# Kernel optimization log

Measured on AMD Instinct MI355X. Metric: run time of the kernel, lower is better.

The kernel has to match this reference:

```python
import jax, jax.numpy as jnp
import numpy as np

L = 8      # subsequence_len
A = 4      # alphabet_size
D = 256    # sketch_dim
SEQ = 16384


def setup_inputs() -> dict:
    key = jax.random.key(0)
    k1, k2, k3 = jax.random.split(key, 3)
    sequence = jax.random.randint(k1, (SEQ,), 0, A)
    # stacked nn.Embedding weights: (L, A, D), init N(0, 0.5)
    hash_emb = 0.5 * jax.random.normal(k2, (L, A, D), dtype=jnp.float32)
    sign_logits = 0.5 * jax.random.normal(k3, (L, A), dtype=jnp.float32)
    return {"sequence": sequence, "hash_emb": hash_emb, "sign_logits": sign_logits}


def _forward(sequence, hash_emb, sign_logits):
    # roll_idx[j, s] = (j - s) % D  so that gather reproduces torch.roll(t, s)[j] = t[(j - s) % D]
    roll_idx = (jnp.arange(D)[:, None] - jnp.arange(D)[None, :]) % D
    p_arr = jnp.arange(1, L + 1, dtype=jnp.float32)           # p = 1..L
    Tp0 = jnp.zeros((L + 1, D), dtype=jnp.float32).at[0, 0].set(1.0)
    Tm0 = jnp.zeros((L + 1, D), dtype=jnp.float32)

    def step(carry, xs):
        Tp, Tm = carry                                         # (L+1, D) each
        c, i = xs
        valid = (c >= 0) & (c < A)
        c_safe = jnp.clip(c, 0, A - 1)
        # eval-mode soft hash: softmax over the embedding row (per level p)
        probs = jax.nn.softmax(hash_emb[:, c_safe, :], axis=-1)   # (L, D)
        sign = jax.nn.sigmoid(sign_logits[:, c_safe])             # (L,)
        denom = (i + 1).astype(jnp.float32)
        # z = p/(i+1); levels with p > i+1 (and invalid chars) are frozen (z=0)
        z = jnp.where((p_arr <= denom) & valid, p_arr / denom, 0.0)  # (L,)
        Tp_prev, Tm_prev = Tp[:L], Tm[:L]                         # (L, D)
        # expected circular shift: out[l, j] = sum_s probs[l, s] * T_prev[l, (j-s)%D]
        stp = jnp.einsum('ljs,ls->lj', Tp_prev[:, roll_idx], probs)
        stm = jnp.einsum('ljs,ls->lj', Tm_prev[:, roll_idx], probs)
        s = sign[:, None]
        upd_p = s * stp + (1.0 - s) * stm
        upd_m = s * stm + (1.0 - s) * stp
        zc = z[:, None]
        new_Tp = Tp.at[1:].set((1.0 - zc) * Tp[1:] + zc * upd_p)
        new_Tm = Tm.at[1:].set((1.0 - zc) * Tm[1:] + zc * upd_m)
        return (new_Tp, new_Tm), None

    step = jax.checkpoint(step)
    (Tp, Tm), _ = jax.lax.scan(step, (Tp0, Tm0), (sequence, jnp.arange(SEQ)))
    return Tp[L] - Tm[L]


def reference(sequence, hash_emb, sign_logits):
    return _forward(sequence, hash_emb, sign_logits)
```

## Files before the change

kernel.cpp:

```cpp
#include <hip/hip_runtime.h>
#include <math.h>

#define LL 8
#define AA 4
#define DD 256
#define KF 129
#define KH 128
#define CLEN 32
#define NGR 128
#define NES 36
#define LPAD 37

typedef float v2f __attribute__((ext_vector_type(2)));

#define SIX(l2,l1) ((((l2)*((l2)-1))>>1) + (l1))
#define SLOT(s)    ((s)*LPAD + ((s)>>1))

#define Q_OFF   0
#define OPS_OFF (32*KF*2)
#define OPS_SZ  (KH*NGR*NES*2)
#define VH_OFF  (OPS_OFF + OPS_SZ)
#define V_OFF   (VH_OFF + 2*40)
#define CNT_OFF (V_OFF + 2*KF)

__device__ __forceinline__ float invCN8() {
  constexpr double c = (16384.0 * 16383.0 * 16382.0 * 16381.0 *
                        16380.0 * 16379.0 * 16378.0 * 16377.0) / 40320.0;
  return (float)(1.0 / c);
}

__device__ __forceinline__ v2f cfma(const v2f b, const v2f a, v2f acc) {
  const v2f bb = (v2f){ b.x,  b.x};
  const v2f bw = (v2f){-b.y,  b.y};
  const v2f as = (v2f){ a.y,  a.x};
  acc = __builtin_elementwise_fma(bb, a,  acc);
  acc = __builtin_elementwise_fma(bw, as, acc);
  return acc;
}

__global__ __launch_bounds__(256) void kq(const float* __restrict__ hemb,
                                          const float* __restrict__ slog,
                                          float* __restrict__ Q,
                                          int* __restrict__ cnt) {
  const int b = blockIdx.x;
  const int t = threadIdx.x;
  if (b == 0 && t == 0) {
    __hip_atomic_store(&cnt[0], 0, __ATOMIC_RELEASE, __HIP_MEMORY_SCOPE_AGENT);
    __hip_atomic_store(&cnt[1], 0, __ATOMIC_RELEASE, __HIP_MEMORY_SCOPE_AGENT);
  }
  __shared__ float sh[DD];
  __shared__ float red[256];
  __shared__ float2 tw[256];
  {
    float sn, cs;
    __sincosf((float)t * (-0.0245436926061702596754894014319f), &sn, &cs);
    tw[t] = make_float2(cs, sn);
  }
  float h = hemb[b * DD + t];
  red[t] = h; __syncthreads();
  for (int off = 128; off > 0; off >>= 1) {
    if (t < off) red[t] = fmaxf(red[t], red[t + off]);
    __syncthreads();
  }
  float mx = red[0]; __syncthreads();
  float e = expf(h - mx);
  red[t] = e; __syncthreads();
  for (int off = 128; off > 0; off >>= 1) {
    if (t < off) red[t] += red[t + off];
    __syncthreads();
  }
  float s = red[0];
  sh[t] = e / s;
  __syncthreads();
  if (t < KF) {
    float cr = 0.0f, ci = 0.0f;
    for (int j = 0; j < DD; ++j) {
      const int m = (t * j) & 255;
      const float2 w = tw[m];
      const float p = sh[j];
      cr = fmaf(p, w.x, cr);
      ci = fmaf(p, w.y, ci);
    }
    const float sl = slog[b];
    const float sg = 1.0f / (1.0f + expf(-sl));
    const float q = fmaf(2.0f, sg, -1.0f);
    Q[(b * KF + t) * 2 + 0] = q * cr;
    Q[(b * KF + t) * 2 + 1] = q * ci;
  }
}

template <int CC>
__device__ __forceinline__ void tstep2(v2f (&G)[NES],
                                       const v2f (&QA)[LL][AA], const v2f (&QB)[LL][AA]) {
#pragma unroll
  for (int l = LL; l >= 1; --l) {
    const v2f qa = QA[l - 1][CC];
    const v2f qb = QB[l - 1][CC];
    {
      v2f g = G[SIX(l, l - 1)];
      g.x += qa.x; g.y += qb.y;
      G[SIX(l, l - 1)] = g;
    }
#pragma unroll
    for (int l1 = 0; l1 < l - 1; ++l1) {
      const v2f H  = G[SIX(l - 1, l1)];
      const v2f Hs = (v2f){H.y, H.x};
      v2f g = G[SIX(l, l1)];
      g = __builtin_elementwise_fma(qa, H,  g);
      g = __builtin_elementwise_fma(qb, Hs, g);
      G[SIX(l, l1)] = g;
    }
  }
}

template <unsigned MASK>
__device__ __forceinline__ void prodCols(const v2f* __restrict__ A, const v2f* __restrict__ B,
                                         v2f (&o)[NES]) {
#pragma unroll
  for (int l1 = 0; l1 < 8; ++l1) {
    if ((MASK >> l1) & 1) {
#pragma unroll
      for (int l2 = l1 + 1; l2 <= 8; ++l2) {
        v2f acc = A[SIX(l2, l1)] + B[SIX(l2, l1)];
#pragma unroll
        for (int m = l1 + 1; m < l2; ++m) acc = cfma(B[SIX(l2, m)], A[SIX(m, l1)], acc);
        o[SIX(l2, l1)] = acc;
      }
    }
  }
}

template <unsigned MASK>
__device__ __forceinline__ void writeCols(v2f* __restrict__ D, const v2f (&o)[NES]) {
#pragma unroll
  for (int l1 = 0; l1 < 8; ++l1) {
    if ((MASK >> l1) & 1) {
#pragma unroll
      for (int l2 = l1 + 1; l2 <= 8; ++l2) D[SIX(l2, l1)] = o[SIX(l2, l1)];
    }
  }
}

__device__ __forceinline__ void prodR(const float* __restrict__ A, const float* __restrict__ B,
                                      float (&o)[NES]) {
#pragma unroll
  for (int l1 = 0; l1 < 8; ++l1) {
#pragma unroll
    for (int l2 = l1 + 1; l2 <= 8; ++l2) {
      float acc = A[SIX(l2, l1)] + B[SIX(l2, l1)];
#pragma unroll
      for (int m = l1 + 1; m < l2; ++m) acc = fmaf(B[SIX(l2, m)], A[SIX(m, l1)], acc);
      o[SIX(l2, l1)] = acc;
    }
  }
}

__global__ __launch_bounds__(256, 1) void kchunk(const int* __restrict__ seq,
                                                 const float* __restrict__ Q,
                                                 float* __restrict__ opsT) {
  const int blk  = blockIdx.x;
  const int g    = blk >> 1;
  const int half = blk & 1;
  const int t    = threadIdx.x;
  const int w    = t >> 6;
  const int lane = t & 63;
  const int k    = half * 64 + lane;

  __shared__ __align__(16) float shb[2 * 64 * LPAD * 2];
  v2f* S0 = (v2f*)shb;
  v2f* S1 = S0 + 64 * LPAD;

  v2f QA[LL][AA], QB[LL][AA];
  const float2* Q2 = (const float2*)Q;
#pragma unroll
  for (int lc = 0; lc < LL * AA; ++lc) {
    const float2 q = Q2[lc * KF + k];
    QA[lc >> 2][lc & 3] = (v2f){ q.x, q.x};
    QB[lc >> 2][lc & 3] = (v2f){-q.y, q.y};
  }

  v2f G[NES];
#pragma unroll
  for (int e = 0; e < NES; ++e) G[e] = (v2f){0.f, 0.f};

  const int chunk = g * 4 + w;
  const int base  = chunk * CLEN;
  const int myc   = seq[base + (lane & 31)];
  for (int s2 = 0; s2 < CLEN; ++s2) {
    const int c = __builtin_amdgcn_readlane(myc, s2);
    switch (c) {
      case 0:  tstep2<0>(G, QA, QB); break;
      case 1:  tstep2<1>(G, QA, QB); break;
      case 2:  tstep2<2>(G, QA, QB); break;
      default: tstep2<3>(G, QA, QB); break;
    }
  }

  const v2f* Ab = S0 + lane * LPAD;
  const v2f* Bb = S1 + lane * LPAD;
  v2f* Db = S0 + lane * LPAD;
  v2f* Wb = S1 + lane * LPAD;
  v2f pc[NES];

  if (w == 0)      { for (int e = 0; e < NES; ++e) Db[e] = G[e]; }
  else if (w == 1) { for (int e = 0; e < NES; ++e) Wb[e] = G[e]; }
  __syncthreads();

  for (int r = 0; r < 3; ++r) {
    switch (w) {
      case 0:  prodCols<0x01>(Ab, Bb, pc); break;
      case 1:  prodCols<0x42>(Ab, Bb, pc); break;
      case 2:  prodCols<0x14>(Ab, Bb, pc); break;
      default: prodCols<0xA8>(Ab, Bb, pc); break;
    }
    __syncthreads();
    switch (w) {
      case 0:  writeCols<0x01>(Db, pc); break;
      case 1:  writeCols<0x42>(Db, pc); break;
      case 2:  writeCols<0x14>(Db, pc); break;
      default: writeCols<0xA8>(Db, pc); break;
    }
    if ((r == 0 && w == 2) || (r == 1 && w == 3)) {
      for (int e = 0; e < NES; ++e) Wb[e] = G[e];
    }
    __syncthreads();
  }

  float2* dst = (float2*)opsT;
  for (int it = 0; it < 9; ++it) {
    const int idx = it * 256 + t;
    const int o   = idx / 36;
    const int e   = idx - o * 36;
    const v2f x   = S0[o * LPAD + e];
    dst[((size_t)(half * 64 + o) * NGR + g) * NES + e] = make_float2(x.x, x.y);
  }
}

__global__ __launch_bounds__(256, 1) void kreduce(const float* __restrict__ opsT,
                                                  const int* __restrict__ seq,
                                                  const float* __restrict__ Q,
                                                  float* __restrict__ vh,
                                                  float* __restrict__ v,
                                                  int* __restrict__ cnt,
                                                  float* __restrict__ outp) {
  const int blk = blockIdx.x;
  const int t   = threadIdx.x;
  __shared__ __align__(16) float ldsf[9600];

  if (blk < KH) {
    const int k = blk;
    v2f* L = (v2f*)ldsf;
    const float4* src4 = (const float4*)(opsT + (size_t)k * NGR * NES * 2);
    for (int it = 0; it < 9; ++it) {
      const int idx = it * 256 + t;
      const float4 x = src4[idx];
      const int o = idx / 18;
      const int u = idx - o * 18;
      L[SLOT(o) + 2 * u]     = (v2f){x.x, x.y};
      L[SLOT(o) + 2 * u + 1] = (v2f){x.z, x.w};
    }
    __syncthreads();

    const int w = t >> 6;
    const int j = t & 63;
    v2f pc[NES];
    for (int n = 64; n >= 8; n >>= 1) {
      const bool act = (j < n);
      if (act) {
        const v2f* Ab = L + SLOT(2 * j);
        const v2f* Bb = L + SLOT(2 * j + 1);
        switch (w) {
          case 0:  prodCols<0x01>(Ab, Bb, pc); break;
          case 1:  prodCols<0x42>(Ab, Bb, pc); break;
          case 2:  prodCols<0x14>(Ab, Bb, pc); break;
          default: prodCols<0xA8>(Ab, Bb, pc); break;
        }
      }
      __syncthreads();
      if (act) {
        v2f* Db = L + SLOT(j);
        switch (w) {
          case 0:  writeCols<0x01>(Db, pc); break;
          case 1:  writeCols<0x42>(Db, pc); break;
          case 2:  writeCols<0x14>(Db, pc); break;
          default: writeCols<0xA8>(Db, pc); break;
        }
      }
      __syncthreads();
    }

    if (t < 64) {
      v2f sv[LL + 1];
      sv[0] = (v2f){1.f, 0.f};
#pragma unroll
      for (int l = 1; l <= LL; ++l) sv[l] = (v2f){0.f, 0.f};
      for (int gg = 0; gg < 8; ++gg) {
        v2f nv = (v2f){0.f, 0.f};
        if (t >= 1 && t <= LL) {
          nv = sv[t];
          const v2f* Bb = L + SLOT(gg);
          const int rb = (t * (t - 1)) >> 1;
#pragma unroll
          for (int l1 = 0; l1 < 8; ++l1) {
            if (l1 < t) nv = cfma(Bb[rb + l1], sv[l1], nv);
          }
        }
#pragma unroll
        for (int l = 1; l <= LL; ++l) {
          sv[l].x = __shfl(nv.x, l);
          sv[l].y = __shfl(nv.y, l);
        }
      }
      if (t == 0) {
        __hip_atomic_store(&v[2 * k],     sv[LL].x, __ATOMIC_RELEASE, __HIP_MEMORY_SCOPE_AGENT);
        __hip_atomic_store(&v[2 * k + 1], sv[LL].y, __ATOMIC_RELEASE, __HIP_MEMORY_SCOPE_AGENT);
      }
    }
  } else {
    const int half = blk - KH;
    float* Lr = ldsf;
    float Q8[LL][AA];
#pragma unroll
    for (int lc = 0; lc < LL * AA; ++lc) Q8[lc >> 2][lc & 3] = Q[(lc * KF + KH) * 2];

    float Gr[NES];
#pragma unroll
    for (int e = 0; e < NES; ++e) Gr[e] = 0.f;

    const int base = (half * 256 + t) * CLEN;
    int sym[CLEN];
    {
      const int4* sp = (const int4*)(seq + base);
#pragma unroll
      for (int u = 0; u < CLEN / 4; ++u) {
        const int4 x = sp[u];
        sym[4 * u + 0] = x.x; sym[4 * u + 1] = x.y;
        sym[4 * u + 2] = x.z; sym[4 * u + 3] = x.w;
      }
    }
#pragma unroll
    for (int s2 = 0; s2 < CLEN; ++s2) {
      const int c = sym[s2];
      float Qs[LL];
#pragma unroll
      for (int l = 0; l < LL; ++l) {
        const float qa = (c & 1) ? Q8[l][1] : Q8[l][0];
        const float qb = (c & 1) ? Q8[l][3] : Q8[l][2];
        Qs[l] = (c & 2) ? qb : qa;
      }
#pragma unroll
      for (int l = LL; l >= 1; --l) {
        Gr[SIX(l, l - 1)] += Qs[l - 1];
#pragma unroll
        for (int l1 = 0; l1 < l - 1; ++l1)
          Gr[SIX(l, l1)] = fmaf(Qs[l - 1], Gr[SIX(l - 1, l1)], Gr[SIX(l, l1)]);
      }
    }
#pragma unroll
    for (int e = 0; e < NES; ++e) Lr[t * LPAD + e] = Gr[e];
    __syncthreads();

    float po[NES];
    for (int n = 128; n >= 1; n >>= 1) {
      const bool act = (t < n);
      if (act) prodR(Lr + (2 * t) * LPAD, Lr + (2 * t + 1) * LPAD, po);
      __syncthreads();
      if (act) { for (int e = 0; e < NES; ++e) Lr[t * LPAD + e] = po[e]; }
      __syncthreads();
    }
    if (t < NES)
      __hip_atomic_store(&vh[half * 40 + t], Lr[t], __ATOMIC_RELEASE, __HIP_MEMORY_SCOPE_AGENT);
    __syncthreads();
    if (t == 0) {
      const int o2 = __hip_atomic_fetch_add(&cnt[1], 1, __ATOMIC_ACQ_REL, __HIP_MEMORY_SCOPE_AGENT);
      if (o2 == 1) {
        float h0[LL + 1];
#pragma unroll
        for (int m = 1; m <= LL; ++m)
          h0[m] = __hip_atomic_load(&vh[0 + SIX(m, 0)], __ATOMIC_ACQUIRE, __HIP_MEMORY_SCOPE_AGENT);
        float acc = h0[LL] +
          __hip_atomic_load(&vh[40 + SIX(LL, 0)], __ATOMIC_ACQUIRE, __HIP_MEMORY_SCOPE_AGENT);
#pragma unroll
        for (int m = 1; m <= 7; ++m)
          acc = fmaf(__hip_atomic_load(&vh[40 + SIX(LL, m)], __ATOMIC_ACQUIRE, __HIP_MEMORY_SCOPE_AGENT),
                     h0[m], acc);
        __hip_atomic_store(&v[2 * KH],     acc,  __ATOMIC_RELEASE, __HIP_MEMORY_SCOPE_AGENT);
        __hip_atomic_store(&v[2 * KH + 1], 0.0f, __ATOMIC_RELEASE, __HIP_MEMORY_SCOPE_AGENT);
      }
    }
  }

  __shared__ int isLast;
  __syncthreads();
  if (t == 0) {
    const int old = __hip_atomic_fetch_add(&cnt[0], 1, __ATOMIC_ACQ_REL, __HIP_MEMORY_SCOPE_AGENT);
    isLast = (old == 129) ? 1 : 0;
  }
  __syncthreads();
  if (isLast) {
    __shared__ float2 twd[256];
    __shared__ float dvr[KF], dvi[KF];
    {
      float sn, cs;
      __sincosf((float)t * 0.0245436926061702596754894014319f, &sn, &cs);
      twd[t] = make_float2(cs, sn);
    }
    if (t < KF) {
      dvr[t] = __hip_atomic_load(&v[2 * t],     __ATOMIC_ACQUIRE, __HIP_MEMORY_SCOPE_AGENT);
      dvi[t] = __hip_atomic_load(&v[2 * t + 1], __ATOMIC_ACQUIRE, __HIP_MEMORY_SCOPE_AGENT);
    }
    if (t == 0) {
      __hip_atomic_store(&cnt[0], 0, __ATOMIC_RELEASE, __HIP_MEMORY_SCOPE_AGENT);
      __hip_atomic_store(&cnt[1], 0, __ATOMIC_RELEASE, __HIP_MEMORY_SCOPE_AGENT);
    }
    __syncthreads();
    const float sc = (1.0f / 256.0f) * invCN8();
    float sum = dvr[0] + ((t & 1) ? -dvr[KH] : dvr[KH]);
    for (int k2 = 1; k2 < KH; ++k2) {
      const int m = (t * k2) & 255;
      const float2 wv = twd[m];
      sum = fmaf(2.0f * dvr[k2], wv.x, sum);
      sum = fmaf(-2.0f * dvi[k2], wv.y, sum);
    }
    outp[t] = sum * sc;
  }
}

extern "C" void kernel_launch(void* const* d_in, const int* in_sizes, int n_in,
                              void* d_out, int out_size, void* d_ws, size_t ws_size,
                              hipStream_t stream) {
  (void)in_sizes; (void)n_in; (void)out_size; (void)ws_size;
  const int*   seq  = (const int*)d_in[0];
  const float* hemb = (const float*)d_in[1];
  const float* slog = (const float*)d_in[2];
  float* ws   = (float*)d_ws;
  float* Q    = ws + Q_OFF;
  float* opsT = ws + OPS_OFF;
  float* vh   = ws + VH_OFF;
  float* v    = ws + V_OFF;
  int*   cnt  = (int*)(ws + CNT_OFF);
  float* o    = (float*)d_out;

  hipLaunchKernelGGL(kq,      dim3(LL * AA), dim3(256), 0, stream, hemb, slog, Q, cnt);
  hipLaunchKernelGGL(kchunk,  dim3(256),     dim3(256), 0, stream, seq, Q, opsT);
  hipLaunchKernelGGL(kreduce, dim3(130),     dim3(256), 0, stream, opsT, seq, Q, vh, v, cnt, o);
}
```

Measured before the change: 105.7 us.

## Fuse three kernels into one cooperative kernel with grid syncs

Merges the Q-transform, chunk-scan and reduction kernels into a single cooperative launch of 256 blocks, separated by grid.sync() barriers. The goal is to remove two kernel launch boundaries and their launch latency. In exchange, every block waits at each grid barrier, including blocks with no work in phases one and three. Shared memory is now reused across phases, and the single launch relies on cooperative-launch support and full co-residency of all blocks.

```diff
diff --git a/kernel.cpp b/kernel.cpp
--- a/kernel.cpp
+++ b/kernel.cpp
@@ -1,5 +1,8 @@
 #include <hip/hip_runtime.h>
+#include <hip/hip_cooperative_groups.h>
 #include <math.h>
+
+namespace cg = cooperative_groups;
 
 #define LL 8
 #define AA 4
@@ -38,57 +41,6 @@
   return acc;
 }
 
-__global__ __launch_bounds__(256) void kq(const float* __restrict__ hemb,
-                                          const float* __restrict__ slog,
-                                          float* __restrict__ Q,
-                                          int* __restrict__ cnt) {
-  const int b = blockIdx.x;
-  const int t = threadIdx.x;
-  if (b == 0 && t == 0) {
-    __hip_atomic_store(&cnt[0], 0, __ATOMIC_RELEASE, __HIP_MEMORY_SCOPE_AGENT);
-    __hip_atomic_store(&cnt[1], 0, __ATOMIC_RELEASE, __HIP_MEMORY_SCOPE_AGENT);
-  }
-  __shared__ float sh[DD];
-  __shared__ float red[256];
-  __shared__ float2 tw[256];
-  {
-    float sn, cs;
-    __sincosf((float)t * (-0.0245436926061702596754894014319f), &sn, &cs);
-    tw[t] = make_float2(cs, sn);
-  }
-  float h = hemb[b * DD + t];
-  red[t] = h; __syncthreads();
-  for (int off = 128; off > 0; off >>= 1) {
-    if (t < off) red[t] = fmaxf(red[t], red[t + off]);
-    __syncthreads();
-  }
-  float mx = red[0]; __syncthreads();
-  float e = expf(h - mx);
-  red[t] = e; __syncthreads();
-  for (int off = 128; off > 0; off >>= 1) {
-    if (t < off) red[t] += red[t + off];
-    __syncthreads();
-  }
-  float s = red[0];
-  sh[t] = e / s;
-  __syncthreads();
-  if (t < KF) {
-    float cr = 0.0f, ci = 0.0f;
-    for (int j = 0; j < DD; ++j) {
-      const int m = (t * j) & 255;
-      const float2 w = tw[m];
-      const float p = sh[j];
-      cr = fmaf(p, w.x, cr);
-      ci = fmaf(p, w.y, ci);
-    }
-    const float sl = slog[b];
-    const float sg = 1.0f / (1.0f + expf(-sl));
-    const float q = fmaf(2.0f, sg, -1.0f);
-    Q[(b * KF + t) * 2 + 0] = q * cr;
-    Q[(b * KF + t) * 2 + 1] = q * ci;
-  }
-}
-
 template <int CC>
 __device__ __forceinline__ void tstep2(v2f (&G)[NES],
                                        const v2f (&QA)[LL][AA], const v2f (&QB)[LL][AA]) {
@@ -155,274 +107,328 @@
   }
 }
 
-__global__ __launch_bounds__(256, 1) void kchunk(const int* __restrict__ seq,
-                                                 const float* __restrict__ Q,
-                                                 float* __restrict__ opsT) {
-  const int blk  = blockIdx.x;
-  const int g    = blk >> 1;
-  const int half = blk & 1;
-  const int t    = threadIdx.x;
-  const int w    = t >> 6;
-  const int lane = t & 63;
-  const int k    = half * 64 + lane;
-
-  __shared__ __align__(16) float shb[2 * 64 * LPAD * 2];
-  v2f* S0 = (v2f*)shb;
-  v2f* S1 = S0 + 64 * LPAD;
-
-  v2f QA[LL][AA], QB[LL][AA];
-  const float2* Q2 = (const float2*)Q;
-#pragma unroll
-  for (int lc = 0; lc < LL * AA; ++lc) {
-    const float2 q = Q2[lc * KF + k];
-    QA[lc >> 2][lc & 3] = (v2f){ q.x, q.x};
-    QB[lc >> 2][lc & 3] = (v2f){-q.y, q.y};
-  }
-
-  v2f G[NES];
-#pragma unroll
-  for (int e = 0; e < NES; ++e) G[e] = (v2f){0.f, 0.f};
-
-  const int chunk = g * 4 + w;
-  const int base  = chunk * CLEN;
-  const int myc   = seq[base + (lane & 31)];
-  for (int s2 = 0; s2 < CLEN; ++s2) {
-    const int c = __builtin_amdgcn_readlane(myc, s2);
-    switch (c) {
-      case 0:  tstep2<0>(G, QA, QB); break;
-      case 1:  tstep2<1>(G, QA, QB); break;
-      case 2:  tstep2<2>(G, QA, QB); break;
-      default: tstep2<3>(G, QA, QB); break;
-    }
-  }
-
-  const v2f* Ab = S0 + lane * LPAD;
-  const v2f* Bb = S1 + lane * LPAD;
-  v2f* Db = S0 + lane * LPAD;
-  v2f* Wb = S1 + lane * LPAD;
-  v2f pc[NES];
-
-  if (w == 0)      { for (int e = 0; e < NES; ++e) Db[e] = G[e]; }
-  else if (w == 1) { for (int e = 0; e < NES; ++e) Wb[e] = G[e]; }
-  __syncthreads();
-
-  for (int r = 0; r < 3; ++r) {
-    switch (w) {
-      case 0:  prodCols<0x01>(Ab, Bb, pc); break;
-      case 1:  prodCols<0x42>(Ab, Bb, pc); break;
-      case 2:  prodCols<0x14>(Ab, Bb, pc); break;
-      default: prodCols<0xA8>(Ab, Bb, pc); break;
-    }
-    __syncthreads();
-    switch (w) {
-      case 0:  writeCols<0x01>(Db, pc); break;
-      case 1:  writeCols<0x42>(Db, pc); break;
-      case 2:  writeCols<0x14>(Db, pc); break;
-      default: writeCols<0xA8>(Db, pc); break;
-    }
-    if ((r == 0 && w == 2) || (r == 1 && w == 3)) {
-      for (int e = 0; e < NES; ++e) Wb[e] = G[e];
-    }
-    __syncthreads();
-  }
-
-  float2* dst = (float2*)opsT;
-  for (int it = 0; it < 9; ++it) {
-    const int idx = it * 256 + t;
-    const int o   = idx / 36;
-    const int e   = idx - o * 36;
-    const v2f x   = S0[o * LPAD + e];
-    dst[((size_t)(half * 64 + o) * NGR + g) * NES + e] = make_float2(x.x, x.y);
-  }
-}
-
-__global__ __launch_bounds__(256, 1) void kreduce(const float* __restrict__ opsT,
-                                                  const int* __restrict__ seq,
-                                                  const float* __restrict__ Q,
-                                                  float* __restrict__ vh,
-                                                  float* __restrict__ v,
-                                                  int* __restrict__ cnt,
-                                                  float* __restrict__ outp) {
+__global__ __launch_bounds__(256, 1) void kfused(const int* __restrict__ seq,
+                                                 const float* __restrict__ hemb,
+                                                 const float* __restrict__ slog,
+                                                 float* __restrict__ Q,
+                                                 float* __restrict__ opsT,
+                                                 float* __restrict__ vh,
+                                                 float* __restrict__ v,
+                                                 int* __restrict__ cnt,
+                                                 float* __restrict__ outp) {
+  cg::grid_group grid = cg::this_grid();
   const int blk = blockIdx.x;
   const int t   = threadIdx.x;
   __shared__ __align__(16) float ldsf[9600];
 
-  if (blk < KH) {
-    const int k = blk;
-    v2f* L = (v2f*)ldsf;
-    const float4* src4 = (const float4*)(opsT + (size_t)k * NGR * NES * 2);
+  if (blk == 0 && t == 0) {
+    __hip_atomic_store(&cnt[0], 0, __ATOMIC_RELEASE, __HIP_MEMORY_SCOPE_AGENT);
+    __hip_atomic_store(&cnt[1], 0, __ATOMIC_RELEASE, __HIP_MEMORY_SCOPE_AGENT);
+  }
+
+  if (blk < LL * AA) {
+    const int b = blk;
+    float*  sh  = ldsf;
+    float*  red = ldsf + 256;
+    float2* tw  = (float2*)(ldsf + 512);
+    {
+      float sn, cs;
+      __sincosf((float)t * (-0.0245436926061702596754894014319f), &sn, &cs);
+      tw[t] = make_float2(cs, sn);
+    }
+    float h = hemb[b * DD + t];
+    red[t] = h; __syncthreads();
+    for (int off = 128; off > 0; off >>= 1) {
+      if (t < off) red[t] = fmaxf(red[t], red[t + off]);
+      __syncthreads();
+    }
+    float mx = red[0]; __syncthreads();
+    float e = expf(h - mx);
+    red[t] = e; __syncthreads();
+    for (int off = 128; off > 0; off >>= 1) {
+      if (t < off) red[t] += red[t + off];
+      __syncthreads();
+    }
+    float s = red[0];
+    sh[t] = e / s;
+    __syncthreads();
+    if (t < KF) {
+      float cr = 0.0f, ci = 0.0f;
+      for (int j = 0; j < DD; ++j) {
+        const int m = (t * j) & 255;
+        const float2 w = tw[m];
+        const float p = sh[j];
+        cr = fmaf(p, w.x, cr);
+        ci = fmaf(p, w.y, ci);
+      }
+      const float sl = slog[b];
+      const float sg = 1.0f / (1.0f + expf(-sl));
+      const float q = fmaf(2.0f, sg, -1.0f);
+      Q[(b * KF + t) * 2 + 0] = q * cr;
+      Q[(b * KF + t) * 2 + 1] = q * ci;
+    }
+    __syncthreads();
+  }
+
+  grid.sync();
+
+  {
+    const int g    = blk >> 1;
+    const int half = blk & 1;
+    const int w    = t >> 6;
+    const int lane = t & 63;
+    const int k    = half * 64 + lane;
+
+    v2f* S0 = (v2f*)ldsf;
+    v2f* S1 = S0 + 64 * LPAD;
+
+    v2f QA[LL][AA], QB[LL][AA];
+    const float2* Q2 = (const float2*)Q;
+#pragma unroll
+    for (int lc = 0; lc < LL * AA; ++lc) {
+      const float2 q = Q2[lc * KF + k];
+      QA[lc >> 2][lc & 3] = (v2f){ q.x, q.x};
+      QB[lc >> 2][lc & 3] = (v2f){-q.y, q.y};
+    }
+
+    v2f G[NES];
+#pragma unroll
+    for (int e = 0; e < NES; ++e) G[e] = (v2f){0.f, 0.f};
+
+    const int chunk = g * 4 + w;
+    const int base  = chunk * CLEN;
+    const int myc   = seq[base + (lane & 31)];
+    for (int s2 = 0; s2 < CLEN; ++s2) {
+      const int c = __builtin_amdgcn_readlane(myc, s2);
+      switch (c) {
+        case 0:  tstep2<0>(G, QA, QB); break;
+        case 1:  tstep2<1>(G, QA, QB); break;
+        case 2:  tstep2<2>(G, QA, QB); break;
+        default: tstep2<3>(G, QA, QB); break;
+      }
+    }
+
+    const v2f* Ab = S0 + lane * LPAD;
+    const v2f* Bb = S1 + lane * LPAD;
+    v2f* Db = S0 + lane * LPAD;
+    v2f* Wb = S1 + lane * LPAD;
+    v2f pc[NES];
+
+    if (w == 0)      { for (int e = 0; e < NES; ++e) Db[e] = G[e]; }
+    else if (w == 1) { for (int e = 0; e < NES; ++e) Wb[e] = G[e]; }
+    __syncthreads();
+
+    for (int r = 0; r < 3; ++r) {
+      switch (w) {
+        case 0:  prodCols<0x01>(Ab, Bb, pc); break;
+        case 1:  prodCols<0x42>(Ab, Bb, pc); break;
+        case 2:  prodCols<0x14>(Ab, Bb, pc); break;
+        default: prodCols<0xA8>(Ab, Bb, pc); break;
+      }
+      __syncthreads();
+      switch (w) {
+        case 0:  writeCols<0x01>(Db, pc); break;
+        case 1:  writeCols<0x42>(Db, pc); break;
+        case 2:  writeCols<0x14>(Db, pc); break;
+        default: writeCols<0xA8>(Db, pc); break;
+      }
+      if ((r == 0 && w == 2) || (r == 1 && w == 3)) {
+        for (int e = 0; e < NES; ++e) Wb[e] = G[e];
+      }
+      __syncthreads();
+    }
+
+    float2* dst = (float2*)opsT;
     for (int it = 0; it < 9; ++it) {
       const int idx = it * 256 + t;
-      const float4 x = src4[idx];
-      const int o = idx / 18;
-      const int u = idx - o * 18;
-      L[SLOT(o) + 2 * u]     = (v2f){x.x, x.y};
-      L[SLOT(o) + 2 * u + 1] = (v2f){x.z, x.w};
-    }
-    __syncthreads();
-
-    const int w = t >> 6;
-    const int j = t & 63;
-    v2f pc[NES];
-    for (int n = 64; n >= 8; n >>= 1) {
-      const bool act = (j < n);
-      if (act) {
-        const v2f* Ab = L + SLOT(2 * j);
-        const v2f* Bb = L + SLOT(2 * j + 1);
-        switch (w) {
-          case 0:  prodCols<0x01>(Ab, Bb, pc); break;
-          case 1:  prodCols<0x42>(Ab, Bb, pc); break;
-          case 2:  prodCols<0x14>(Ab, Bb, pc); break;
-          default: prodCols<0xA8>(Ab, Bb, pc); break;
-        }
-      }
-      __syncthreads();
-      if (act) {
-        v2f* Db = L + SLOT(j);
-        switch (w) {
-          case 0:  writeCols<0x01>(Db, pc); break;
-          case 1:  writeCols<0x42>(Db, pc); break;
-          case 2:  writeCols<0x14>(Db, pc); break;
-          default: writeCols<0xA8>(Db, pc); break;
-        }
-      }
-      __syncthreads();
-    }
-
-    if (t < 64) {
-      v2f sv[LL + 1];
-      sv[0] = (v2f){1.f, 0.f};
-#pragma unroll
-      for (int l = 1; l <= LL; ++l) sv[l] = (v2f){0.f, 0.f};
-      for (int gg = 0; gg < 8; ++gg) {
-        v2f nv = (v2f){0.f, 0.f};
-        if (t >= 1 && t <= LL) {
-          nv = sv[t];
-          const v2f* Bb = L + SLOT(gg);
-          const int rb = (t * (t - 1)) >> 1;
-#pragma unroll
-          for (int l1 = 0; l1 < 8; ++l1) {
-            if (l1 < t) nv = cfma(Bb[rb + l1], sv[l1], nv);
+      const int o   = idx / 36;
+      const int e   = idx - o * 36;
+      const v2f x   = S0[o * LPAD + e];
+      dst[((size_t)(half * 64 + o) * NGR + g) * NES + e] = make_float2(x.x, x.y);
+    }
+    __syncthreads();
+  }
+
+  grid.sync();
+
+  if (blk < KH + 2) {
+    if (blk < KH) {
+      const int k = blk;
+      v2f* L = (v2f*)ldsf;
+      const float4* src4 = (const float4*)(opsT + (size_t)k * NGR * NES * 2);
+      for (int it = 0; it < 9; ++it) {
+        const int idx = it * 256 + t;
+        const float4 x = src4[idx];
+        const int o = idx / 18;
+        const int u = idx - o * 18;
+        L[SLOT(o) + 2 * u]     = (v2f){x.x, x.y};
+        L[SLOT(o) + 2 * u + 1] = (v2f){x.z, x.w};
+      }
+      __syncthreads();
+
+      const int w = t >> 6;
+      const int j = t & 63;
+      v2f pc[NES];
+      for (int n = 64; n >= 8; n >>= 1) {
+        const bool act = (j < n);
+        if (act) {
+          const v2f* Ab = L + SLOT(2 * j);
+          const v2f* Bb = L + SLOT(2 * j + 1);
+          switch (w) {
+            case 0:  prodCols<0x01>(Ab, Bb, pc); break;
+            case 1:  prodCols<0x42>(Ab, Bb, pc); break;
+            case 2:  prodCols<0x14>(Ab, Bb, pc); break;
+            default: prodCols<0xA8>(Ab, Bb, pc); break;
           }
         }
-#pragma unroll
-        for (int l = 1; l <= LL; ++l) {
-          sv[l].x = __shfl(nv.x, l);
-          sv[l].y = __shfl(nv.y, l);
-        }
-      }
+        __syncthreads();
+        if (act) {
+          v2f* Db = L + SLOT(j);
+          switch (w) {
+            case 0:  writeCols<0x01>(Db, pc); break;
+            case 1:  writeCols<0x42>(Db, pc); break;
+            case 2:  writeCols<0x14>(Db, pc); break;
+            default: writeCols<0xA8>(Db, pc); break;
+          }
+        }
+        __syncthreads();
+      }
+
+      if (t < 64) {
+        v2f sv[LL + 1];
+        sv[0] = (v2f){1.f, 0.f};
+#pragma unroll
+        for (int l = 1; l <= LL; ++l) sv[l] = (v2f){0.f, 0.f};
+        for (int gg = 0; gg < 8; ++gg) {
+          v2f nv = (v2f){0.f, 0.f};
+          if (t >= 1 && t <= LL) {
+            nv = sv[t];
+            const v2f* Bb = L + SLOT(gg);
+            const int rb = (t * (t - 1)) >> 1;
+#pragma unroll
+            for (int l1 = 0; l1 < 8; ++l1) {
+              if (l1 < t) nv = cfma(Bb[rb + l1], sv[l1], nv);
+            }
+          }
+#pragma unroll
+          for (int l = 1; l <= LL; ++l) {
+            sv[l].x = __shfl(nv.x, l);
+            sv[l].y = __shfl(nv.y, l);
+          }
+        }
+        if (t == 0) {
+          __hip_atomic_store(&v[2 * k],     sv[LL].x, __ATOMIC_RELEASE, __HIP_MEMORY_SCOPE_AGENT);
+          __hip_atomic_store(&v[2 * k + 1], sv[LL].y, __ATOMIC_RELEASE, __HIP_MEMORY_SCOPE_AGENT);
+        }
+      }
+    } else {
+      const int half = blk - KH;
+      float* Lr = ldsf;
+      float Q8[LL][AA];
+#pragma unroll
+      for (int lc = 0; lc < LL * AA; ++lc) Q8[lc >> 2][lc & 3] = Q[(lc * KF + KH) * 2];
+
+      float Gr[NES];
+#pragma unroll
+      for (int e = 0; e < NES; ++e) Gr[e] = 0.f;
+
+      const int base = (half * 256 + t) * CLEN;
+      int sym[CLEN];
+      {
+        const int4* sp = (const int4*)(seq + base);
+#pragma unroll
+        for (int u = 0; u < CLEN / 4; ++u) {
+          const int4 x = sp[u];
+          sym[4 * u + 0] = x.x; sym[4 * u + 1] = x.y;
+          sym[4 * u + 2] = x.z; sym[4 * u + 3] = x.w;
+        }
+      }
+#pragma unroll
+      for (int s2 = 0; s2 < CLEN; ++s2) {
+        const int c = sym[s2];
+        float Qs[LL];
+#pragma unroll
+        for (int l = 0; l < LL; ++l) {
+          const float qa = (c & 1) ? Q8[l][1] : Q8[l][0];
+          const float qb = (c & 1) ? Q8[l][3] : Q8[l][2];
+          Qs[l] = (c & 2) ? qb : qa;
+        }
+#pragma unroll
+        for (int l = LL; l >= 1; --l) {
+          Gr[SIX(l, l - 1)] += Qs[l - 1];
+#pragma unroll
+          for (int l1 = 0; l1 < l - 1; ++l1)
+            Gr[SIX(l, l1)] = fmaf(Qs[l - 1], Gr[SIX(l - 1, l1)], Gr[SIX(l, l1)]);
+        }
+      }
+#pragma unroll
+      for (int e = 0; e < NES; ++e) Lr[t * LPAD + e] = Gr[e];
+      __syncthreads();
+
+      float po[NES];
+      for (int n = 128; n >= 1; n >>= 1) {
+        const bool act = (t < n);
+        if (act) prodR(Lr + (2 * t) * LPAD, Lr + (2 * t + 1) * LPAD, po);
+        __syncthreads();
+        if (act) { for (int e = 0; e < NES; ++e) Lr[t * LPAD + e] = po[e]; }
+        __syncthreads();
+      }
+      if (t < NES)
+        __hip_atomic_store(&vh[half * 40 + t], Lr[t], __ATOMIC_RELEASE, __HIP_MEMORY_SCOPE_AGENT);
+      __syncthreads();
       if (t == 0) {
-        __hip_atomic_store(&v[2 * k],     sv[LL].x, __ATOMIC_RELEASE, __HIP_MEMORY_SCOPE_AGENT);
-        __hip_atomic_store(&v[2 * k + 1], sv[LL].y, __ATOMIC_RELEASE, __HIP_MEMORY_SCOPE_AGENT);
-      }
-    }
-  } else {
-    const int half = blk - KH;
-    float* Lr = ldsf;
-    float Q8[LL][AA];
-#pragma unroll
-    for (int lc = 0; lc < LL * AA; ++lc) Q8[lc >> 2][lc & 3] = Q[(lc * KF + KH) * 2];
-
-    float Gr[NES];
-#pragma unroll
-    for (int e = 0; e < NES; ++e) Gr[e] = 0.f;
-
-    const int base = (half * 256 + t) * CLEN;
-    int sym[CLEN];
-    {
-      const int4* sp = (const int4*)(seq + base);
-#pragma unroll
-      for (int u = 0; u < CLEN / 4; ++u) {
-        const int4 x = sp[u];
-        sym[4 * u + 0] = x.x; sym[4 * u + 1] = x.y;
-        sym[4 * u + 2] = x.z; sym[4 * u + 3] = x.w;
-      }
-    }
-#pragma unroll
-    for (int s2 = 0; s2 < CLEN; ++s2) {
-      const int c = sym[s2];
-      float Qs[LL];
-#pragma unroll
-      for (int l = 0; l < LL; ++l) {
-        const float qa = (c & 1) ? Q8[l][1] : Q8[l][0];
-        const float qb = (c & 1) ? Q8[l][3] : Q8[l][2];
-        Qs[l] = (c & 2) ? qb : qa;
-      }
-#pragma unroll
-      for (int l = LL; l >= 1; --l) {
-        Gr[SIX(l, l - 1)] += Qs[l - 1];
-#pragma unroll
-        for (int l1 = 0; l1 < l - 1; ++l1)
-          Gr[SIX(l, l1)] = fmaf(Qs[l - 1], Gr[SIX(l - 1, l1)], Gr[SIX(l, l1)]);
-      }
-    }
-#pragma unroll
-    for (int e = 0; e < NES; ++e) Lr[t * LPAD + e] = Gr[e];
-    __syncthreads();
-
-    float po[NES];
-    for (int n = 128; n >= 1; n >>= 1) {
-      const bool act = (t < n);
-      if (act) prodR(Lr + (2 * t) * LPAD, Lr + (2 * t + 1) * LPAD, po);
-      __syncthreads();
-      if (act) { for (int e = 0; e < NES; ++e) Lr[t * LPAD + e] = po[e]; }
-      __syncthreads();
-    }
-    if (t < NES)
-      __hip_atomic_store(&vh[half * 40 + t], Lr[t], __ATOMIC_RELEASE, __HIP_MEMORY_SCOPE_AGENT);
+        const int o2 = __hip_atomic_fetch_add(&cnt[1], 1, __ATOMIC_ACQ_REL, __HIP_MEMORY_SCOPE_AGENT);
+        if (o2 == 1) {
+          float h0[LL + 1];
+#pragma unroll
+          for (int m = 1; m <= LL; ++m)
+            h0[m] = __hip_atomic_load(&vh[0 + SIX(m, 0)], __ATOMIC_ACQUIRE, __HIP_MEMORY_SCOPE_AGENT);
+          float acc = h0[LL] +
+            __hip_atomic_load(&vh[40 + SIX(LL, 0)], __ATOMIC_ACQUIRE, __HIP_MEMORY_SCOPE_AGENT);
+#pragma unroll
+          for (int m = 1; m <= 7; ++m)
+            acc = fmaf(__hip_atomic_load(&vh[40 + SIX(LL, m)], __ATOMIC_ACQUIRE, __HIP_MEMORY_SCOPE_AGENT),
+                       h0[m], acc);
+          __hip_atomic_store(&v[2 * KH],     acc,  __ATOMIC_RELEASE, __HIP_MEMORY_SCOPE_AGENT);
+          __hip_atomic_store(&v[2 * KH + 1], 0.0f, __ATOMIC_RELEASE, __HIP_MEMORY_SCOPE_AGENT);
+        }
+      }
+    }
+
+    __shared__ int isLast;
     __syncthreads();
     if (t == 0) {
-      const int o2 = __hip_atomic_fetch_add(&cnt[1], 1, __ATOMIC_ACQ_REL, __HIP_MEMORY_SCOPE_AGENT);
-      if (o2 == 1) {
-        float h0[LL + 1];
-#pragma unroll
-        for (int m = 1; m <= LL; ++m)
-          h0[m] = __hip_atomic_load(&vh[0 + SIX(m, 0)], __ATOMIC_ACQUIRE, __HIP_MEMORY_SCOPE_AGENT);
-        float acc = h0[LL] +
-          __hip_atomic_load(&vh[40 + SIX(LL, 0)], __ATOMIC_ACQUIRE, __HIP_MEMORY_SCOPE_AGENT);
-#pragma unroll
-        for (int m = 1; m <= 7; ++m)
-          acc = fmaf(__hip_atomic_load(&vh[40 + SIX(LL, m)], __ATOMIC_ACQUIRE, __HIP_MEMORY_SCOPE_AGENT),
-                     h0[m], acc);
-        __hip_atomic_store(&v[2 * KH],     acc,  __ATOMIC_RELEASE, __HIP_MEMORY_SCOPE_AGENT);
-        __hip_atomic_store(&v[2 * KH + 1], 0.0f, __ATOMIC_RELEASE, __HIP_MEMORY_SCOPE_AGENT);
-      }
-    }
-  }
-
-  __shared__ int isLast;
-  __syncthreads();
-  if (t == 0) {
-    const int old = __hip_atomic_fetch_add(&cnt[0], 1, __ATOMIC_ACQ_REL, __HIP_MEMORY_SCOPE_AGENT);
-    isLast = (old == 129) ? 1 : 0;
-  }
-  __syncthreads();
-  if (isLast) {
-    __shared__ float2 twd[256];
-    __shared__ float dvr[KF], dvi[KF];
-    {
-      float sn, cs;
-      __sincosf((float)t * 0.0245436926061702596754894014319f, &sn, &cs);
-      twd[t] = make_float2(cs, sn);
-    }
-    if (t < KF) {
-      dvr[t] = __hip_atomic_load(&v[2 * t],     __ATOMIC_ACQUIRE, __HIP_MEMORY_SCOPE_AGENT);
-      dvi[t] = __hip_atomic_load(&v[2 * t + 1], __ATOMIC_ACQUIRE, __HIP_MEMORY_SCOPE_AGENT);
-    }
-    if (t == 0) {
-      __hip_atomic_store(&cnt[0], 0, __ATOMIC_RELEASE, __HIP_MEMORY_SCOPE_AGENT);
-      __hip_atomic_store(&cnt[1], 0, __ATOMIC_RELEASE, __HIP_MEMORY_SCOPE_AGENT);
-    }
-    __syncthreads();
-    const float sc = (1.0f / 256.0f) * invCN8();
-    float sum = dvr[0] + ((t & 1) ? -dvr[KH] : dvr[KH]);
-    for (int k2 = 1; k2 < KH; ++k2) {
-      const int m = (t * k2) & 255;
-      const float2 wv = twd[m];
-      sum = fmaf(2.0f * dvr[k2], wv.x, sum);
-      sum = fmaf(-2.0f * dvi[k2], wv.y, sum);
-    }
-    outp[t] = sum * sc;
+      const int old = __hip_atomic_fetch_add(&cnt[0], 1, __ATOMIC_ACQ_REL, __HIP_MEMORY_SCOPE_AGENT);
+      isLast = (old == KH + 1) ? 1 : 0;
+    }
+    __syncthreads();
+    if (isLast) {
+      __shared__ float2 twd[256];
+      __shared__ float dvr[KF], dvi[KF];
+      {
+        float sn, cs;
+        __sincosf((float)t * 0.0245436926061702596754894014319f, &sn, &cs);
+        twd[t] = make_float2(cs, sn);
+      }
+      if (t < KF) {
+        dvr[t] = __hip_atomic_load(&v[2 * t],     __ATOMIC_ACQUIRE, __HIP_MEMORY_SCOPE_AGENT);
+        dvi[t] = __hip_atomic_load(&v[2 * t + 1], __ATOMIC_ACQUIRE, __HIP_MEMORY_SCOPE_AGENT);
+      }
+      if (t == 0) {
+        __hip_atomic_store(&cnt[0], 0, __ATOMIC_RELEASE, __HIP_MEMORY_SCOPE_AGENT);
+        __hip_atomic_store(&cnt[1], 0, __ATOMIC_RELEASE, __HIP_MEMORY_SCOPE_AGENT);
+      }
+      __syncthreads();
+      const float sc = (1.0f / 256.0f) * invCN8();
+      float sum = dvr[0] + ((t & 1) ? -dvr[KH] : dvr[KH]);
+      for (int k2 = 1; k2 < KH; ++k2) {
+        const int m = (t * k2) & 255;
+        const float2 wv = twd[m];
+        sum = fmaf(2.0f * dvr[k2], wv.x, sum);
+        sum = fmaf(-2.0f * dvi[k2], wv.y, sum);
+      }
+      outp[t] = sum * sc;
+    }
   }
 }
 
@@ -441,7 +447,7 @@
   int*   cnt  = (int*)(ws + CNT_OFF);
   float* o    = (float*)d_out;
 
-  hipLaunchKernelGGL(kq,      dim3(LL * AA), dim3(256), 0, stream, hemb, slog, Q, cnt);
-  hipLaunchKernelGGL(kchunk,  dim3(256),     dim3(256), 0, stream, seq, Q, opsT);
-  hipLaunchKernelGGL(kreduce, dim3(130),     dim3(256), 0, stream, opsT, seq, Q, vh, v, cnt, o);
-}
+  void* args[] = { (void*)&seq, (void*)&hemb, (void*)&slog, (void*)&Q, (void*)&opsT,
+                   (void*)&vh, (void*)&v, (void*)&cnt, (void*)&o };
+  hipLaunchCooperativeKernel((const void*)kfused, dim3(256), dim3(256), args, 0, stream);
+}
```

Result: slower. 166.8 us (+57.9%).

## Fuse chunk scan into reduce kernel, one block per frequency with longer chunks

Applied to the files above, without the earlier changes.

Removes the separate chunk kernel and its global intermediate buffer. Each of the 128 frequency blocks now scans the whole sequence itself, with 256 threads each handling 64 symbols using a Q table in shared memory. Adjacent thread pairs combine in registers before the shared-memory tree reduction. The real-valued Nyquist block now covers the full sequence alone, which drops the two-half combine step and the second counter. This saves one launch and the global round trip, but the scan now runs on 129 blocks instead of 256 and reads Q through LDS with data-dependent indexing.

```diff
diff --git a/kernel.cpp b/kernel.cpp
--- a/kernel.cpp
+++ b/kernel.cpp
@@ -6,8 +6,8 @@
 #define DD 256
 #define KF 129
 #define KH 128
-#define CLEN 32
-#define NGR 128
+#define CLEN 64
+#define NCH 256
 #define NES 36
 #define LPAD 37
 
@@ -17,10 +17,7 @@
 #define SLOT(s)    ((s)*LPAD + ((s)>>1))
 
 #define Q_OFF   0
-#define OPS_OFF (32*KF*2)
-#define OPS_SZ  (KH*NGR*NES*2)
-#define VH_OFF  (OPS_OFF + OPS_SZ)
-#define V_OFF   (VH_OFF + 2*40)
+#define V_OFF   (32*KF*2)
 #define CNT_OFF (V_OFF + 2*KF)
 
 __device__ __forceinline__ float invCN8() {
@@ -38,16 +35,70 @@
   return acc;
 }
 
+template <unsigned MASK>
+__device__ __forceinline__ void prodCols(const v2f* __restrict__ A, const v2f* __restrict__ B,
+                                         v2f (&o)[NES]) {
+#pragma unroll
+  for (int l1 = 0; l1 < 8; ++l1) {
+    if ((MASK >> l1) & 1) {
+#pragma unroll
+      for (int l2 = l1 + 1; l2 <= 8; ++l2) {
+        v2f acc = A[SIX(l2, l1)] + B[SIX(l2, l1)];
+#pragma unroll
+        for (int m = l1 + 1; m < l2; ++m) acc = cfma(B[SIX(l2, m)], A[SIX(m, l1)], acc);
+        o[SIX(l2, l1)] = acc;
+      }
+    }
+  }
+}
+
+template <unsigned MASK>
+__device__ __forceinline__ void writeCols(v2f* __restrict__ D, const v2f (&o)[NES]) {
+#pragma unroll
+  for (int l1 = 0; l1 < 8; ++l1) {
+    if ((MASK >> l1) & 1) {
+#pragma unroll
+      for (int l2 = l1 + 1; l2 <= 8; ++l2) D[SIX(l2, l1)] = o[SIX(l2, l1)];
+    }
+  }
+}
+
+__device__ __forceinline__ void prodFullRA(const v2f (&A)[NES], const v2f* __restrict__ B,
+                                           v2f (&o)[NES]) {
+#pragma unroll
+  for (int l1 = 0; l1 < 8; ++l1) {
+#pragma unroll
+    for (int l2 = l1 + 1; l2 <= 8; ++l2) {
+      v2f acc = A[SIX(l2, l1)] + B[SIX(l2, l1)];
+#pragma unroll
+      for (int m = l1 + 1; m < l2; ++m) acc = cfma(B[SIX(l2, m)], A[SIX(m, l1)], acc);
+      o[SIX(l2, l1)] = acc;
+    }
+  }
+}
+
+__device__ __forceinline__ void prodR(const float* __restrict__ A, const float* __restrict__ B,
+                                      float (&o)[NES]) {
+#pragma unroll
+  for (int l1 = 0; l1 < 8; ++l1) {
+#pragma unroll
+    for (int l2 = l1 + 1; l2 <= 8; ++l2) {
+      float acc = A[SIX(l2, l1)] + B[SIX(l2, l1)];
+#pragma unroll
+      for (int m = l1 + 1; m < l2; ++m) acc = fmaf(B[SIX(l2, m)], A[SIX(m, l1)], acc);
+      o[SIX(l2, l1)] = acc;
+    }
+  }
+}
+
 __global__ __launch_bounds__(256) void kq(const float* __restrict__ hemb,
                                           const float* __restrict__ slog,
                                           float* __restrict__ Q,
                                           int* __restrict__ cnt) {
   const int b = blockIdx.x;
   const int t = threadIdx.x;
-  if (b == 0 && t == 0) {
+  if (b == 0 && t == 0)
     __hip_atomic_store(&cnt[0], 0, __ATOMIC_RELEASE, __HIP_MEMORY_SCOPE_AGENT);
-    __hip_atomic_store(&cnt[1], 0, __ATOMIC_RELEASE, __HIP_MEMORY_SCOPE_AGENT);
-  }
   __shared__ float sh[DD];
   __shared__ float red[256];
   __shared__ float2 tw[256];
@@ -89,175 +140,75 @@
   }
 }
 
-template <int CC>
-__device__ __forceinline__ void tstep2(v2f (&G)[NES],
-                                       const v2f (&QA)[LL][AA], const v2f (&QB)[LL][AA]) {
-#pragma unroll
-  for (int l = LL; l >= 1; --l) {
-    const v2f qa = QA[l - 1][CC];
-    const v2f qb = QB[l - 1][CC];
-    {
-      v2f g = G[SIX(l, l - 1)];
-      g.x += qa.x; g.y += qb.y;
-      G[SIX(l, l - 1)] = g;
-    }
-#pragma unroll
-    for (int l1 = 0; l1 < l - 1; ++l1) {
-      const v2f H  = G[SIX(l - 1, l1)];
-      const v2f Hs = (v2f){H.y, H.x};
-      v2f g = G[SIX(l, l1)];
-      g = __builtin_elementwise_fma(qa, H,  g);
-      g = __builtin_elementwise_fma(qb, Hs, g);
-      G[SIX(l, l1)] = g;
-    }
-  }
-}
-
-template <unsigned MASK>
-__device__ __forceinline__ void prodCols(const v2f* __restrict__ A, const v2f* __restrict__ B,
-                                         v2f (&o)[NES]) {
-#pragma unroll
-  for (int l1 = 0; l1 < 8; ++l1) {
-    if ((MASK >> l1) & 1) {
-#pragma unroll
-      for (int l2 = l1 + 1; l2 <= 8; ++l2) {
-        v2f acc = A[SIX(l2, l1)] + B[SIX(l2, l1)];
-#pragma unroll
-        for (int m = l1 + 1; m < l2; ++m) acc = cfma(B[SIX(l2, m)], A[SIX(m, l1)], acc);
-        o[SIX(l2, l1)] = acc;
-      }
-    }
-  }
-}
-
-template <unsigned MASK>
-__device__ __forceinline__ void writeCols(v2f* __restrict__ D, const v2f (&o)[NES]) {
-#pragma unroll
-  for (int l1 = 0; l1 < 8; ++l1) {
-    if ((MASK >> l1) & 1) {
-#pragma unroll
-      for (int l2 = l1 + 1; l2 <= 8; ++l2) D[SIX(l2, l1)] = o[SIX(l2, l1)];
-    }
-  }
-}
-
-__device__ __forceinline__ void prodR(const float* __restrict__ A, const float* __restrict__ B,
-                                      float (&o)[NES]) {
-#pragma unroll
-  for (int l1 = 0; l1 < 8; ++l1) {
-#pragma unroll
-    for (int l2 = l1 + 1; l2 <= 8; ++l2) {
-      float acc = A[SIX(l2, l1)] + B[SIX(l2, l1)];
-#pragma unroll
-      for (int m = l1 + 1; m < l2; ++m) acc = fmaf(B[SIX(l2, m)], A[SIX(m, l1)], acc);
-      o[SIX(l2, l1)] = acc;
-    }
-  }
-}
-
-__global__ __launch_bounds__(256, 1) void kchunk(const int* __restrict__ seq,
-                                                 const float* __restrict__ Q,
-                                                 float* __restrict__ opsT) {
-  const int blk  = blockIdx.x;
-  const int g    = blk >> 1;
-  const int half = blk & 1;
-  const int t    = threadIdx.x;
-  const int w    = t >> 6;
-  const int lane = t & 63;
-  const int k    = half * 64 + lane;
-
-  __shared__ __align__(16) float shb[2 * 64 * LPAD * 2];
-  v2f* S0 = (v2f*)shb;
-  v2f* S1 = S0 + 64 * LPAD;
-
-  v2f QA[LL][AA], QB[LL][AA];
-  const float2* Q2 = (const float2*)Q;
-#pragma unroll
-  for (int lc = 0; lc < LL * AA; ++lc) {
-    const float2 q = Q2[lc * KF + k];
-    QA[lc >> 2][lc & 3] = (v2f){ q.x, q.x};
-    QB[lc >> 2][lc & 3] = (v2f){-q.y, q.y};
-  }
-
-  v2f G[NES];
-#pragma unroll
-  for (int e = 0; e < NES; ++e) G[e] = (v2f){0.f, 0.f};
-
-  const int chunk = g * 4 + w;
-  const int base  = chunk * CLEN;
-  const int myc   = seq[base + (lane & 31)];
-  for (int s2 = 0; s2 < CLEN; ++s2) {
-    const int c = __builtin_amdgcn_readlane(myc, s2);
-    switch (c) {
-      case 0:  tstep2<0>(G, QA, QB); break;
-      case 1:  tstep2<1>(G, QA, QB); break;
-      case 2:  tstep2<2>(G, QA, QB); break;
-      default: tstep2<3>(G, QA, QB); break;
-    }
-  }
-
-  const v2f* Ab = S0 + lane * LPAD;
-  const v2f* Bb = S1 + lane * LPAD;
-  v2f* Db = S0 + lane * LPAD;
-  v2f* Wb = S1 + lane * LPAD;
-  v2f pc[NES];
-
-  if (w == 0)      { for (int e = 0; e < NES; ++e) Db[e] = G[e]; }
-  else if (w == 1) { for (int e = 0; e < NES; ++e) Wb[e] = G[e]; }
-  __syncthreads();
-
-  for (int r = 0; r < 3; ++r) {
-    switch (w) {
-      case 0:  prodCols<0x01>(Ab, Bb, pc); break;
-      case 1:  prodCols<0x42>(Ab, Bb, pc); break;
-      case 2:  prodCols<0x14>(Ab, Bb, pc); break;
-      default: prodCols<0xA8>(Ab, Bb, pc); break;
-    }
-    __syncthreads();
-    switch (w) {
-      case 0:  writeCols<0x01>(Db, pc); break;
-      case 1:  writeCols<0x42>(Db, pc); break;
-      case 2:  writeCols<0x14>(Db, pc); break;
-      default: writeCols<0xA8>(Db, pc); break;
-    }
-    if ((r == 0 && w == 2) || (r == 1 && w == 3)) {
-      for (int e = 0; e < NES; ++e) Wb[e] = G[e];
-    }
-    __syncthreads();
-  }
-
-  float2* dst = (float2*)opsT;
-  for (int it = 0; it < 9; ++it) {
-    const int idx = it * 256 + t;
-    const int o   = idx / 36;
-    const int e   = idx - o * 36;
-    const v2f x   = S0[o * LPAD + e];
-    dst[((size_t)(half * 64 + o) * NGR + g) * NES + e] = make_float2(x.x, x.y);
-  }
-}
-
-__global__ __launch_bounds__(256, 1) void kreduce(const float* __restrict__ opsT,
-                                                  const int* __restrict__ seq,
-                                                  const float* __restrict__ Q,
-                                                  float* __restrict__ vh,
-                                                  float* __restrict__ v,
-                                                  int* __restrict__ cnt,
-                                                  float* __restrict__ outp) {
+__global__ __launch_bounds__(256, 1) void kmain(const int* __restrict__ seq,
+                                                const float* __restrict__ Q,
+                                                float* __restrict__ v,
+                                                int* __restrict__ cnt,
+                                                float* __restrict__ outp) {
   const int blk = blockIdx.x;
   const int t   = threadIdx.x;
   __shared__ __align__(16) float ldsf[9600];
+  __shared__ __align__(16) float4 qtab[LL * AA];
 
   if (blk < KH) {
     const int k = blk;
+    const float2* Q2 = (const float2*)Q;
+    if (t < LL * AA) {
+      const float2 q = Q2[t * KF + k];
+      qtab[t] = make_float4(q.x, q.x, -q.y, q.y);
+    }
+    __syncthreads();
+
+    v2f G[NES];
+#pragma unroll
+    for (int e = 0; e < NES; ++e) G[e] = (v2f){0.f, 0.f};
+
+    const int4* sp = (const int4*)(seq + t * CLEN);
+    for (int sb = 0; sb < CLEN / 4; ++sb) {
+      const int4 cs = sp[sb];
+      const int csy[4] = {cs.x, cs.y, cs.z, cs.w};
+#pragma unroll
+      for (int u = 0; u < 4; ++u) {
+        const int c = csy[u];
+        float4 qv[LL];
+#pragma unroll
+        for (int l = 0; l < LL; ++l) qv[l] = qtab[(l << 2) | c];
+#pragma unroll
+        for (int l = LL; l >= 1; --l) {
+          const float4 q4 = qv[l - 1];
+          const v2f qa = (v2f){q4.x, q4.y};
+          const v2f qb = (v2f){q4.z, q4.w};
+          {
+            v2f g = G[SIX(l, l - 1)];
+            g.x += q4.x; g.y += q4.w;
+            G[SIX(l, l - 1)] = g;
+          }
+#pragma unroll
+          for (int l1 = 0; l1 < l - 1; ++l1) {
+            const v2f H  = G[SIX(l - 1, l1)];
+            const v2f Hs = (v2f){H.y, H.x};
+            v2f g = G[SIX(l, l1)];
+            g = __builtin_elementwise_fma(qa, H,  g);
+            g = __builtin_elementwise_fma(qb, Hs, g);
+            G[SIX(l, l1)] = g;
+          }
+        }
+      }
+    }
+
     v2f* L = (v2f*)ldsf;
-    const float4* src4 = (const float4*)(opsT + (size_t)k * NGR * NES * 2);
-    for (int it = 0; it < 9; ++it) {
-      const int idx = it * 256 + t;
-      const float4 x = src4[idx];
-      const int o = idx / 18;
-      const int u = idx - o * 18;
-      L[SLOT(o) + 2 * u]     = (v2f){x.x, x.y};
-      L[SLOT(o) + 2 * u + 1] = (v2f){x.z, x.w};
+    if (t & 1) {
+      v2f* D = L + SLOT(t >> 1);
+#pragma unroll
+      for (int e = 0; e < NES; ++e) D[e] = G[e];
+    }
+    __syncthreads();
+    if (!(t & 1)) {
+      v2f o[NES];
+      prodFullRA(G, L + SLOT(t >> 1), o);
+      v2f* D = L + SLOT(t >> 1);
+#pragma unroll
+      for (int e = 0; e < NES; ++e) D[e] = o[e];
     }
     __syncthreads();
 
@@ -317,7 +268,6 @@
       }
     }
   } else {
-    const int half = blk - KH;
     float* Lr = ldsf;
     float Q8[LL][AA];
 #pragma unroll
@@ -327,33 +277,27 @@
 #pragma unroll
     for (int e = 0; e < NES; ++e) Gr[e] = 0.f;
 
-    const int base = (half * 256 + t) * CLEN;
-    int sym[CLEN];
-    {
-      const int4* sp = (const int4*)(seq + base);
-#pragma unroll
-      for (int u = 0; u < CLEN / 4; ++u) {
-        const int4 x = sp[u];
-        sym[4 * u + 0] = x.x; sym[4 * u + 1] = x.y;
-        sym[4 * u + 2] = x.z; sym[4 * u + 3] = x.w;
-      }
-    }
-#pragma unroll
-    for (int s2 = 0; s2 < CLEN; ++s2) {
-      const int c = sym[s2];
-      float Qs[LL];
-#pragma unroll
-      for (int l = 0; l < LL; ++l) {
-        const float qa = (c & 1) ? Q8[l][1] : Q8[l][0];
-        const float qb = (c & 1) ? Q8[l][3] : Q8[l][2];
-        Qs[l] = (c & 2) ? qb : qa;
-      }
-#pragma unroll
-      for (int l = LL; l >= 1; --l) {
-        Gr[SIX(l, l - 1)] += Qs[l - 1];
-#pragma unroll
-        for (int l1 = 0; l1 < l - 1; ++l1)
-          Gr[SIX(l, l1)] = fmaf(Qs[l - 1], Gr[SIX(l - 1, l1)], Gr[SIX(l, l1)]);
+    const int4* sp = (const int4*)(seq + t * CLEN);
+    for (int sb = 0; sb < CLEN / 4; ++sb) {
+      const int4 cs = sp[sb];
+      const int csy[4] = {cs.x, cs.y, cs.z, cs.w};
+#pragma unroll
+      for (int u = 0; u < 4; ++u) {
+        const int c = csy[u];
+        float Qs[LL];
+#pragma unroll
+        for (int l = 0; l < LL; ++l) {
+          const float qa = (c & 1) ? Q8[l][1] : Q8[l][0];
+          const float qb = (c & 1) ? Q8[l][3] : Q8[l][2];
+          Qs[l] = (c & 2) ? qb : qa;
+        }
+#pragma unroll
+        for (int l = LL; l >= 1; --l) {
+          Gr[SIX(l, l - 1)] += Qs[l - 1];
+#pragma unroll
+          for (int l1 = 0; l1 < l - 1; ++l1)
+            Gr[SIX(l, l1)] = fmaf(Qs[l - 1], Gr[SIX(l - 1, l1)], Gr[SIX(l, l1)]);
+        }
       }
     }
 #pragma unroll
@@ -368,25 +312,9 @@
       if (act) { for (int e = 0; e < NES; ++e) Lr[t * LPAD + e] = po[e]; }
       __syncthreads();
     }
-    if (t < NES)
-      __hip_atomic_store(&vh[half * 40 + t], Lr[t], __ATOMIC_RELEASE, __HIP_MEMORY_SCOPE_AGENT);
-    __syncthreads();
     if (t == 0) {
-      const int o2 = __hip_atomic_fetch_add(&cnt[1], 1, __ATOMIC_ACQ_REL, __HIP_MEMORY_SCOPE_AGENT);
-      if (o2 == 1) {
-        float h0[LL + 1];
-#pragma unroll
-        for (int m = 1; m <= LL; ++m)
-          h0[m] = __hip_atomic_load(&vh[0 + SIX(m, 0)], __ATOMIC_ACQUIRE, __HIP_MEMORY_SCOPE_AGENT);
-        float acc = h0[LL] +
-          __hip_atomic_load(&vh[40 + SIX(LL, 0)], __ATOMIC_ACQUIRE, __HIP_MEMORY_SCOPE_AGENT);
-#pragma unroll
-        for (int m = 1; m <= 7; ++m)
-          acc = fmaf(__hip_atomic_load(&vh[40 + SIX(LL, m)], __ATOMIC_ACQUIRE, __HIP_MEMORY_SCOPE_AGENT),
-                     h0[m], acc);
-        __hip_atomic_store(&v[2 * KH],     acc,  __ATOMIC_RELEASE, __HIP_MEMORY_SCOPE_AGENT);
-        __hip_atomic_store(&v[2 * KH + 1], 0.0f, __ATOMIC_RELEASE, __HIP_MEMORY_SCOPE_AGENT);
-      }
+      __hip_atomic_store(&v[2 * KH],     Lr[SIX(LL, 0)], __ATOMIC_RELEASE, __HIP_MEMORY_SCOPE_AGENT);
+      __hip_atomic_store(&v[2 * KH + 1], 0.0f,           __ATOMIC_RELEASE, __HIP_MEMORY_SCOPE_AGENT);
     }
   }
 
@@ -394,7 +322,7 @@
   __syncthreads();
   if (t == 0) {
     const int old = __hip_atomic_fetch_add(&cnt[0], 1, __ATOMIC_ACQ_REL, __HIP_MEMORY_SCOPE_AGENT);
-    isLast = (old == 129) ? 1 : 0;
+    isLast = (old == KH) ? 1 : 0;
   }
   __syncthreads();
   if (isLast) {
@@ -411,7 +339,6 @@
     }
     if (t == 0) {
       __hip_atomic_store(&cnt[0], 0, __ATOMIC_RELEASE, __HIP_MEMORY_SCOPE_AGENT);
-      __hip_atomic_store(&cnt[1], 0, __ATOMIC_RELEASE, __HIP_MEMORY_SCOPE_AGENT);
     }
     __syncthreads();
     const float sc = (1.0f / 256.0f) * invCN8();
@@ -435,13 +362,10 @@
   const float* slog = (const float*)d_in[2];
   float* ws   = (float*)d_ws;
   float* Q    = ws + Q_OFF;
-  float* opsT = ws + OPS_OFF;
-  float* vh   = ws + VH_OFF;
   float* v    = ws + V_OFF;
   int*   cnt  = (int*)(ws + CNT_OFF);
   float* o    = (float*)d_out;
 
-  hipLaunchKernelGGL(kq,      dim3(LL * AA), dim3(256), 0, stream, hemb, slog, Q, cnt);
-  hipLaunchKernelGGL(kchunk,  dim3(256),     dim3(256), 0, stream, seq, Q, opsT);
-  hipLaunchKernelGGL(kreduce, dim3(130),     dim3(256), 0, stream, opsT, seq, Q, vh, v, cnt, o);
-}
+  hipLaunchKernelGGL(kq,    dim3(LL * AA), dim3(256), 0, stream, hemb, slog, Q, cnt);
+  hipLaunchKernelGGL(kmain, dim3(KF),      dim3(256), 0, stream, seq, Q, v, cnt, o);
+}
```

Measured after the change: 98.46 us. 6.8% less time.
